# Kernel tuning notes

Measured on AMD Instinct MI355X. Metric: run time of the kernel, lower is better.

The kernel has to match this reference:

```python
import jax, jax.numpy as jnp
import numpy as np

N_NODES = 100_000
N_EDGES = 1_600_000
HIDDEN = 64
EPS = 1e-5  # eqx.nn.RMSNorm default eps


def setup_inputs() -> dict:
    key = jax.random.key(0)
    k1, k2, k3 = jax.random.split(key, 3)
    x = jax.random.normal(k1, (N_NODES, HIDDEN), dtype=jnp.float32)
    # edges[0] = target node i, edges[1] = source node j  (a[i, j] = 1 => edge j -> i)
    edges = jax.random.randint(k2, (2, N_EDGES), 0, N_NODES, dtype=jnp.int32)
    W = jax.random.normal(k3, (HIDDEN, HIDDEN), dtype=jnp.float32) * (1.0 / np.sqrt(HIDDEN))
    b = jnp.zeros((HIDDEN,), dtype=jnp.float32)
    norm_weight = jnp.ones((HIDDEN,), dtype=jnp.float32)
    norm_bias = jnp.zeros((HIDDEN,), dtype=jnp.float32)
    return {"x": x, "edges": edges, "W": W, "b": b,
            "norm_weight": norm_weight, "norm_bias": norm_bias}


def reference(x, edges, W, b, norm_weight, norm_bias):
    n_nodes = x.shape[0]
    # vmap(Linear) + relu:  m = relu(x @ W.T + b)
    m = jax.nn.relu(jnp.einsum('nd,kd->nk', x, W) + b)
    # a @ m : sum-aggregate messages from source j into target i
    dst, src = edges[0], edges[1]
    agg = jax.ops.segment_sum(m[src], dst, num_segments=n_nodes)
    # residual + RMSNorm (per-node)
    h = x + agg
    inv_rms = jax.lax.rsqrt(jnp.mean(h * h, axis=-1, keepdims=True) + EPS)
    return norm_weight * (h * inv_rms) + norm_bias
```

## Files before the change

### kernel.cpp

```cpp
#include <hip/hip_runtime.h>
#include <hip/hip_bf16.h>

#define N_NODES 100000
#define N_EDGES 1600000
#define HID 64

#define NG 196
#define GROUPS 511
#define GSTRIDE 512
#define NREP 2
#define RCAP 2048
#define EPT 16
#define BIN_BLOCKS 391
#define LIN_BLOCKS 1563
#define LCAP 48

using bf16 = __hip_bfloat16;
typedef __attribute__((ext_vector_type(8))) short short8;
typedef __attribute__((ext_vector_type(4))) float float4v;

__device__ __forceinline__ float bfbits2f(unsigned short u) {
    union { unsigned int i; float f; } v;
    v.i = ((unsigned int)u) << 16;
    return v.f;
}
__device__ __forceinline__ unsigned short f2bfbits(float f) {
    union { float f; unsigned int i; } v;
    v.f = f;
    unsigned int r = v.i + 0x7fffu + ((v.i >> 16) & 1u);
    return (unsigned short)(r >> 16);
}

__global__ __launch_bounds__(256) void k_init(
    const float* __restrict__ W, int* __restrict__ gcur,
    unsigned short* __restrict__ Wfhi, unsigned short* __restrict__ Wflo)
{
    const int t = blockIdx.x * 256 + threadIdx.x;
    for (int i = t; i < NREP * GSTRIDE; i += 512) gcur[i] = 0;
    for (int o = t; o < HID * HID; o += 512) {
        const int j = o & 7, l = (o >> 3) & 63, ksnt = o >> 9;
        const int ks = ksnt & 1, nt = ksnt >> 1;
        const int c = l & 15, q = l >> 4;
        const float f = W[(size_t)(nt * 16 + c) * HID + ks * 32 + q * 8 + j];
        const unsigned short h = f2bfbits(f);
        Wfhi[o] = h;
        Wflo[o] = f2bfbits(f - bfbits2f(h));
    }
}

__global__ __launch_bounds__(256, 4) void k_prep2(
    const float* __restrict__ x, const unsigned short* __restrict__ Wfhi,
    const unsigned short* __restrict__ Wflo, const float* __restrict__ b,
    bf16* __restrict__ m,
    const int* __restrict__ edges, int* __restrict__ gcur,
    int* __restrict__ binned)
{
    __shared__ union SM {
        struct { float xs[64 * 65]; } lin;
        struct { int cnt[GSTRIDE]; int base[GSTRIDE]; } bin;
    } sm;
    const int t = threadIdx.x;

    if (blockIdx.x < LIN_BLOCKS) {
        const int nb0 = blockIdx.x * 64;
        const float4* xg = reinterpret_cast<const float4*>(x) + (size_t)nb0 * 16;
        #pragma unroll
        for (int k = 0; k < 4; ++k) {
            const int f4 = t + k * 256;
            float4 v = make_float4(0.f, 0.f, 0.f, 0.f);
            if (nb0 * 16 + f4 < N_NODES * 16) v = xg[f4];
            const int r = f4 >> 4, fc = (f4 & 15) * 4;
            float* dst = &sm.lin.xs[r * 65 + fc];
            dst[0] = v.x; dst[1] = v.y; dst[2] = v.z; dst[3] = v.w;
        }
        __syncthreads();

        const int wv = t >> 6, l = t & 63;
        const int c = l & 15, q = l >> 4;
        const int tile = blockIdx.x * 4 + wv;
        if (tile >= N_NODES / 16) return;
        const int nb = tile * 16;

        const short8* wfh = reinterpret_cast<const short8*>(Wfhi);
        const short8* wfl = reinterpret_cast<const short8*>(Wflo);
        short8 Bhi[4][2], Blo[4][2];
        #pragma unroll
        for (int nt = 0; nt < 4; ++nt)
            #pragma unroll
            for (int ks = 0; ks < 2; ++ks) {
                const int fi = (nt * 2 + ks) * 64 + l;
                Bhi[nt][ks] = wfh[fi];
                Blo[nt][ks] = wfl[fi];
            }

        short8 Ahi[2];
        #pragma unroll
        for (int ks = 0; ks < 2; ++ks) {
            const float* xsrc = &sm.lin.xs[(wv * 16 + c) * 65 + ks * 32 + q * 8];
            #pragma unroll
            for (int j = 0; j < 8; ++j)
                Ahi[ks][j] = (short)f2bfbits(xsrc[j]);
        }

        float4v acc[4];
        #pragma unroll
        for (int nt = 0; nt < 4; ++nt) {
            const float bias = b[nt * 16 + c];
            acc[nt] = (float4v){bias, bias, bias, bias};
            #pragma unroll
            for (int ks = 0; ks < 2; ++ks) {
                acc[nt] = __builtin_amdgcn_mfma_f32_16x16x32_bf16(Ahi[ks], Bhi[nt][ks], acc[nt], 0, 0, 0);
                acc[nt] = __builtin_amdgcn_mfma_f32_16x16x32_bf16(Ahi[ks], Blo[nt][ks], acc[nt], 0, 0, 0);
            }
        }

        unsigned short* mp = reinterpret_cast<unsigned short*>(m);
        #pragma unroll
        for (int nt = 0; nt < 4; ++nt)
            #pragma unroll
            for (int rg = 0; rg < 4; ++rg) {
                const float v = fmaxf(acc[nt][rg], 0.0f);
                mp[(size_t)(nb + q * 4 + rg) * HID + nt * 16 + c] = f2bfbits(v);
            }
    } else {
        int* cnt  = sm.bin.cnt;
        int* base = sm.bin.base;
        const int bb = blockIdx.x - LIN_BLOCKS;
        for (int i = t; i < GSTRIDE; i += 256) cnt[i] = 0;
        __syncthreads();

        const int e0 = bb * (256 * EPT);
        int gk[EPT], pk[EPT], sl[EPT];
        #pragma unroll
        for (int k = 0; k < EPT; ++k) {
            const int e = e0 + k * 256 + t;
            if (e < N_EDGES) {
                const int dst = edges[e];
                const int src = edges[N_EDGES + e];
                const int g = (int)((unsigned)dst / NG);
                gk[k] = g;
                pk[k] = ((dst - g * NG) << 17) | src;
                sl[k] = atomicAdd(&cnt[g], 1);
            } else gk[k] = -1;
        }
        __syncthreads();
        const int r = bb & (NREP - 1);
        for (int i = t; i < GROUPS; i += 256) {
            const int cc = cnt[i];
            base[i] = cc ? atomicAdd(&gcur[r * GSTRIDE + i], cc) : 0;
        }
        __syncthreads();
        #pragma unroll
        for (int k = 0; k < EPT; ++k) {
            if (gk[k] >= 0) {
                const int pos = base[gk[k]] + sl[k];
                if ((unsigned)pos < RCAP)
                    binned[(size_t)(r * GSTRIDE + gk[k]) * RCAP + pos] = pk[k];
            }
        }
    }
}

__global__ __launch_bounds__(1024, 8) void k_gather_norm6(
    const float* __restrict__ x, const bf16* __restrict__ m,
    const int* __restrict__ gcur, const int* __restrict__ binned,
    const float* __restrict__ nw, const float* __restrict__ nb,
    float* __restrict__ out)
{
    __shared__ int lcount[NG];
    __shared__ int lsrc[NG * LCAP];
    const int t = threadIdx.x;
    const int g = blockIdx.x;
    for (int i = t; i < NG; i += 1024) lcount[i] = 0;
    __syncthreads();

    #pragma unroll
    for (int rr = 0; rr < NREP; ++rr) {
        int c = gcur[rr * GSTRIDE + g];
        if (c > RCAP) c = RCAP;
        const int* reg = binned + (size_t)(rr * GSTRIDE + g) * RCAP;
        for (int i = t; i < c; i += 1024) {
            const int pr = reg[i];
            const int dl = pr >> 17;
            const int slot = atomicAdd(&lcount[dl], 1);
            if (slot < LCAP) lsrc[dl * LCAP + slot] = pr & 0x1FFFF;
        }
    }
    __syncthreads();

    const int wv = t >> 6, l = t & 63;
    const int c = l & 15;
    const int r = l >> 4;
    const ushort4* mu4 = reinterpret_cast<const ushort4*>(m);
    const float4 nw4 = reinterpret_cast<const float4*>(nw)[c];
    const float4 nb4 = reinterpret_cast<const float4*>(nb)[c];

    for (int dl = wv; dl < NG; dl += 16) {
        const int n = g * NG + dl;
        if (n >= N_NODES) break;
        int deg = lcount[dl]; if (deg > LCAP) deg = LCAP;
        const int* row = &lsrc[dl * LCAP];

        float4 a = make_float4(0.f, 0.f, 0.f, 0.f);
        for (int i0 = 0; i0 < deg; i0 += 32) {
            ushort4 vb[8];
            #pragma unroll
            for (int j = 0; j < 8; ++j) {
                const int e = i0 + j * 4 + r;
                const int ec = (e < deg) ? e : (deg - 1);
                vb[j] = mu4[(size_t)row[ec] * 16 + c];
            }
            #pragma unroll
            for (int j = 0; j < 8; ++j) {
                const int e = i0 + j * 4 + r;
                if (e < deg) {
                    a.x += bfbits2f(vb[j].x);
                    a.y += bfbits2f(vb[j].y);
                    a.z += bfbits2f(vb[j].z);
                    a.w += bfbits2f(vb[j].w);
                }
            }
        }
        a.x += __shfl_xor(a.x, 16, 64); a.x += __shfl_xor(a.x, 32, 64);
        a.y += __shfl_xor(a.y, 16, 64); a.y += __shfl_xor(a.y, 32, 64);
        a.z += __shfl_xor(a.z, 16, 64); a.z += __shfl_xor(a.z, 32, 64);
        a.w += __shfl_xor(a.w, 16, 64); a.w += __shfl_xor(a.w, 32, 64);

        const float4 x4 = reinterpret_cast<const float4*>(x)[(size_t)n * 16 + c];
        float4 h;
        h.x = x4.x + a.x; h.y = x4.y + a.y; h.z = x4.z + a.z; h.w = x4.w + a.w;
        float ss = h.x * h.x + h.y * h.y + h.z * h.z + h.w * h.w;
        ss += __shfl_xor(ss, 1, 64);
        ss += __shfl_xor(ss, 2, 64);
        ss += __shfl_xor(ss, 4, 64);
        ss += __shfl_xor(ss, 8, 64);
        const float inv = rsqrtf(ss * (1.0f / HID) + 1e-5f);
        if (r == 0) {
            float4 o;
            o.x = nw4.x * h.x * inv + nb4.x;
            o.y = nw4.y * h.y * inv + nb4.y;
            o.z = nw4.z * h.z * inv + nb4.z;
            o.w = nw4.w * h.w * inv + nb4.w;
            reinterpret_cast<float4*>(out)[(size_t)n * 16 + c] = o;
        }
    }
}

extern "C" void kernel_launch(void* const* d_in, const int* in_sizes, int n_in,
                              void* d_out, int out_size, void* d_ws, size_t ws_size,
                              hipStream_t stream) {
    const float* x     = (const float*)d_in[0];
    const int*   edges = (const int*)d_in[1];
    const float* W     = (const float*)d_in[2];
    const float* b     = (const float*)d_in[3];
    const float* nw    = (const float*)d_in[4];
    const float* nb    = (const float*)d_in[5];
    float* out = (float*)d_out;

    int* gcur = (int*)d_ws;
    unsigned short* Wfhi = (unsigned short*)((char*)d_ws + (1 << 14));
    unsigned short* Wflo = Wfhi + HID * HID;
    int*  binned = (int*)((char*)d_ws + (1 << 16));
    bf16* m      = (bf16*)((char*)d_ws + (1 << 16) +
                           (size_t)NREP * GSTRIDE * RCAP * sizeof(int));

    k_init<<<2, 256, 0, stream>>>(W, gcur, Wfhi, Wflo);
    k_prep2<<<LIN_BLOCKS + BIN_BLOCKS, 256, 0, stream>>>(x, Wfhi, Wflo, b, m, edges, gcur, binned);
    k_gather_norm6<<<GROUPS, 1024, 0, stream>>>(x, m, gcur, binned, nw, nb, out);
}
```

Measured before the change: 149.6 us.

## Aggregate neighbor messages with one-hot bf16 MFMA over 16-node tiles

The gather kernel now buckets edges into tiles of 16 destination nodes instead of per-node lists. Each wave loads source message rows as 16-byte vectors, transposes them through LDS with ds_read_b64_tr_b16, and sums them into the destination nodes with a one-hot bf16 MFMA. The goal is to replace per-lane scalar bf16-to-float adds and shuffle reductions with matrix-core accumulation, and to use wider loads. In exchange there is extra LDS staging, padding waste per 32-edge chunk, and a smaller block (768 threads) whose per-tile capacity limit could drop edges.

```diff
diff --git a/kernel.cpp b/kernel.cpp
--- a/kernel.cpp
+++ b/kernel.cpp
@@ -13,10 +13,15 @@
 #define EPT 16
 #define BIN_BLOCKS 391
 #define LIN_BLOCKS 1563
-#define LCAP 48
+
+#define TILES 13
+#define TCAP 384
+#define GTHREADS 768
+#define GWAVES 12
 
 using bf16 = __hip_bfloat16;
 typedef __attribute__((ext_vector_type(8))) short short8;
+typedef __attribute__((ext_vector_type(4))) short short4v;
 typedef __attribute__((ext_vector_type(4))) float float4v;
 
 __device__ __forceinline__ float bfbits2f(unsigned short u) {
@@ -161,17 +166,23 @@
     }
 }
 
-__global__ __launch_bounds__(1024, 8) void k_gather_norm6(
+#define TRREAD(dst, OFF) \
+    asm volatile("ds_read_b64_tr_b16 %0, %1 offset:" #OFF \
+                 : "=v"(dst) : "v"(traddr) : "memory")
+
+__global__ __launch_bounds__(GTHREADS, 6) void k_gather_mfma(
     const float* __restrict__ x, const bf16* __restrict__ m,
     const int* __restrict__ gcur, const int* __restrict__ binned,
-    const float* __restrict__ nw, const float* __restrict__ nb,
+    const float* __restrict__ nw, const float* __restrict__ nbias,
     float* __restrict__ out)
 {
-    __shared__ int lcount[NG];
-    __shared__ int lsrc[NG * LCAP];
+    __shared__ int tcnt[TILES];
+    __shared__ int tlist[TILES * TCAP];
+    __shared__ uint4 stg4[GWAVES * 128];
+
     const int t = threadIdx.x;
     const int g = blockIdx.x;
-    for (int i = t; i < NG; i += 1024) lcount[i] = 0;
+    if (t < TILES) tcnt[t] = 0;
     __syncthreads();
 
     #pragma unroll
@@ -179,69 +190,125 @@
         int c = gcur[rr * GSTRIDE + g];
         if (c > RCAP) c = RCAP;
         const int* reg = binned + (size_t)(rr * GSTRIDE + g) * RCAP;
-        for (int i = t; i < c; i += 1024) {
+        for (int i = t; i < c; i += GTHREADS) {
             const int pr = reg[i];
-            const int dl = pr >> 17;
-            const int slot = atomicAdd(&lcount[dl], 1);
-            if (slot < LCAP) lsrc[dl * LCAP + slot] = pr & 0x1FFFF;
+            const int tile = pr >> 21;
+            const int slot = atomicAdd(&tcnt[tile], 1);
+            if (slot < TCAP) tlist[tile * TCAP + slot] = pr & 0x1FFFFF;
         }
     }
     __syncthreads();
 
     const int wv = t >> 6, l = t & 63;
-    const int c = l & 15;
-    const int r = l >> 4;
-    const ushort4* mu4 = reinterpret_cast<const ushort4*>(m);
-    const float4 nw4 = reinterpret_cast<const float4*>(nw)[c];
-    const float4 nb4 = reinterpret_cast<const float4*>(nb)[c];
-
-    for (int dl = wv; dl < NG; dl += 16) {
+    const int q = l >> 4;
+    const int node16 = l & 15;
+    const int fq = l & 7;
+    const int sr = l >> 3;
+    const int stg_c = ((fq >> 1) << 9) | ((l >> 5) << 7) | ((sr & 3) << 5) | ((l & 1) << 4);
+    const int kq0 = ((sr >> 2) << 3) + (sr & 3);
+    const int kq1 = (((sr + 8) >> 2) << 3) + (sr & 3);
+    char* stg_wave = (char*)(&stg4[0]) + (wv << 11);
+    const unsigned traddr = (unsigned)(size_t)stg_wave + (unsigned)(l << 3);
+    const uint4* mv = reinterpret_cast<const uint4*>(m);
+
+    for (int tile = wv; tile < TILES; tile += GWAVES) {
+        int K = tcnt[tile];
+        if (K > TCAP) K = TCAP;
+        const int lbase = tile * TCAP;
+        float4v acc0 = {0.f, 0.f, 0.f, 0.f};
+        float4v acc1 = acc0, acc2 = acc0, acc3 = acc0;
+        const int nch = (K + 31) >> 5;
+
+        for (int ch = 0; ch < nch; ++ch) {
+            const int k0 = ch << 5;
+            const int kA0 = k0 + kq0, kA1 = k0 + kq1;
+            const int tA0i = (kA0 < K) ? tlist[lbase + kA0] : 0;
+            const int tA1i = (kA1 < K) ? tlist[lbase + kA1] : 0;
+            const int tB0i = (kA0 + 4 < K) ? tlist[lbase + kA0 + 4] : 0;
+            const int tB1i = (kA1 + 4 < K) ? tlist[lbase + kA1 + 4] : 0;
+            const uint4 vA0 = mv[(size_t)(tA0i & 0x1FFFF) * 8 + fq];
+            const uint4 vA1 = mv[(size_t)(tA1i & 0x1FFFF) * 8 + fq];
+            const uint4 vB0 = mv[(size_t)(tB0i & 0x1FFFF) * 8 + fq];
+            const uint4 vB1 = mv[(size_t)(tB1i & 0x1FFFF) * 8 + fq];
+
+            *reinterpret_cast<uint4*>(stg_wave + stg_c) = vA0;
+            *reinterpret_cast<uint4*>(stg_wave + stg_c + 256) = vA1;
+            short4v tA0, tA1, tA2, tA3;
+            TRREAD(tA0, 0); TRREAD(tA1, 512); TRREAD(tA2, 1024); TRREAD(tA3, 1536);
+
+            *reinterpret_cast<uint4*>(stg_wave + stg_c) = vB0;
+            *reinterpret_cast<uint4*>(stg_wave + stg_c + 256) = vB1;
+            short4v tB0, tB1, tB2, tB3;
+            TRREAD(tB0, 0); TRREAD(tB1, 512); TRREAD(tB2, 1024); TRREAD(tB3, 1536);
+
+            const int kb = k0 + (q << 3);
+            short8 bh;
+            #pragma unroll
+            for (int jj = 0; jj < 8; ++jj) {
+                const int kk = kb + jj;
+                const int tb = (kk < K) ? tlist[lbase + kk] : -1;
+                bh[jj] = (short)(((tb >> 17) == node16) ? 0x3F80 : 0);
+            }
+
+            asm volatile("s_waitcnt lgkmcnt(0)" ::: "memory");
+            __builtin_amdgcn_sched_barrier(0);
+            const short8 a0 = __builtin_shufflevector(tA0, tB0, 0, 1, 2, 3, 4, 5, 6, 7);
+            const short8 a1 = __builtin_shufflevector(tA1, tB1, 0, 1, 2, 3, 4, 5, 6, 7);
+            const short8 a2 = __builtin_shufflevector(tA2, tB2, 0, 1, 2, 3, 4, 5, 6, 7);
+            const short8 a3 = __builtin_shufflevector(tA3, tB3, 0, 1, 2, 3, 4, 5, 6, 7);
+            acc0 = __builtin_amdgcn_mfma_f32_16x16x32_bf16(a0, bh, acc0, 0, 0, 0);
+            acc1 = __builtin_amdgcn_mfma_f32_16x16x32_bf16(a1, bh, acc1, 0, 0, 0);
+            acc2 = __builtin_amdgcn_mfma_f32_16x16x32_bf16(a2, bh, acc2, 0, 0, 0);
+            acc3 = __builtin_amdgcn_mfma_f32_16x16x32_bf16(a3, bh, acc3, 0, 0, 0);
+        }
+
+        const int dl = (tile << 4) + node16;
         const int n = g * NG + dl;
-        if (n >= N_NODES) break;
-        int deg = lcount[dl]; if (deg > LCAP) deg = LCAP;
-        const int* row = &lsrc[dl * LCAP];
-
-        float4 a = make_float4(0.f, 0.f, 0.f, 0.f);
-        for (int i0 = 0; i0 < deg; i0 += 32) {
-            ushort4 vb[8];
-            #pragma unroll
-            for (int j = 0; j < 8; ++j) {
-                const int e = i0 + j * 4 + r;
-                const int ec = (e < deg) ? e : (deg - 1);
-                vb[j] = mu4[(size_t)row[ec] * 16 + c];
-            }
-            #pragma unroll
-            for (int j = 0; j < 8; ++j) {
-                const int e = i0 + j * 4 + r;
-                if (e < deg) {
-                    a.x += bfbits2f(vb[j].x);
-                    a.y += bfbits2f(vb[j].y);
-                    a.z += bfbits2f(vb[j].z);
-                    a.w += bfbits2f(vb[j].w);
-                }
-            }
-        }
-        a.x += __shfl_xor(a.x, 16, 64); a.x += __shfl_xor(a.x, 32, 64);
-        a.y += __shfl_xor(a.y, 16, 64); a.y += __shfl_xor(a.y, 32, 64);
-        a.z += __shfl_xor(a.z, 16, 64); a.z += __shfl_xor(a.z, 32, 64);
-        a.w += __shfl_xor(a.w, 16, 64); a.w += __shfl_xor(a.w, 32, 64);
-
-        const float4 x4 = reinterpret_cast<const float4*>(x)[(size_t)n * 16 + c];
-        float4 h;
-        h.x = x4.x + a.x; h.y = x4.y + a.y; h.z = x4.z + a.z; h.w = x4.w + a.w;
-        float ss = h.x * h.x + h.y * h.y + h.z * h.z + h.w * h.w;
-        ss += __shfl_xor(ss, 1, 64);
-        ss += __shfl_xor(ss, 2, 64);
-        ss += __shfl_xor(ss, 4, 64);
-        ss += __shfl_xor(ss, 8, 64);
-        const float inv = rsqrtf(ss * (1.0f / HID) + 1e-5f);
-        if (r == 0) {
-            float4 o;
-            o.x = nw4.x * h.x * inv + nb4.x;
-            o.y = nw4.y * h.y * inv + nb4.y;
-            o.z = nw4.z * h.z * inv + nb4.z;
-            o.w = nw4.w * h.w * inv + nb4.w;
-            reinterpret_cast<float4*>(out)[(size_t)n * 16 + c] = o;
+        if (dl < NG && n < N_NODES) {
+            const float4* xr = reinterpret_cast<const float4*>(x) + (size_t)n * 16 + q;
+            const float4 x0 = xr[0], x1 = xr[4], x2 = xr[8], x3 = xr[12];
+            const float h00 = x0.x + acc0[0], h01 = x0.y + acc0[1], h02 = x0.z + acc0[2], h03 = x0.w + acc0[3];
+            const float h10 = x1.x + acc1[0], h11 = x1.y + acc1[1], h12 = x1.z + acc1[2], h13 = x1.w + acc1[3];
+            const float h20 = x2.x + acc2[0], h21 = x2.y + acc2[1], h22 = x2.z + acc2[2], h23 = x2.w + acc2[3];
+            const float h30 = x3.x + acc3[0], h31 = x3.y + acc3[1], h32 = x3.z + acc3[2], h33 = x3.w + acc3[3];
+            float ss = h00 * h00 + h01 * h01 + h02 * h02 + h03 * h03
+                     + h10 * h10 + h11 * h11 + h12 * h12 + h13 * h13
+                     + h20 * h20 + h21 * h21 + h22 * h22 + h23 * h23
+                     + h30 * h30 + h31 * h31 + h32 * h32 + h33 * h33;
+            ss += __shfl_xor(ss, 16, 64);
+            ss += __shfl_xor(ss, 32, 64);
+            const float inv = rsqrtf(ss * (1.0f / HID) + 1e-5f);
+            const float4* nwp = reinterpret_cast<const float4*>(nw);
+            const float4* nbp = reinterpret_cast<const float4*>(nbias);
+            float4* op = reinterpret_cast<float4*>(out) + (size_t)n * 16 + q;
+            {
+                const float4 w = nwp[q], bb = nbp[q];
+                float4 o;
+                o.x = w.x * h00 * inv + bb.x; o.y = w.y * h01 * inv + bb.y;
+                o.z = w.z * h02 * inv + bb.z; o.w = w.w * h03 * inv + bb.w;
+                op[0] = o;
+            }
+            {
+                const float4 w = nwp[4 + q], bb = nbp[4 + q];
+                float4 o;
+                o.x = w.x * h10 * inv + bb.x; o.y = w.y * h11 * inv + bb.y;
+                o.z = w.z * h12 * inv + bb.z; o.w = w.w * h13 * inv + bb.w;
+                op[4] = o;
+            }
+            {
+                const float4 w = nwp[8 + q], bb = nbp[8 + q];
+                float4 o;
+                o.x = w.x * h20 * inv + bb.x; o.y = w.y * h21 * inv + bb.y;
+                o.z = w.z * h22 * inv + bb.z; o.w = w.w * h23 * inv + bb.w;
+                op[8] = o;
+            }
+            {
+                const float4 w = nwp[12 + q], bb = nbp[12 + q];
+                float4 o;
+                o.x = w.x * h30 * inv + bb.x; o.y = w.y * h31 * inv + bb.y;
+                o.z = w.z * h32 * inv + bb.z; o.w = w.w * h33 * inv + bb.w;
+                op[12] = o;
+            }
         }
     }
 }
@@ -266,5 +333,5 @@
 
     k_init<<<2, 256, 0, stream>>>(W, gcur, Wfhi, Wflo);
     k_prep2<<<LIN_BLOCKS + BIN_BLOCKS, 256, 0, stream>>>(x, Wfhi, Wflo, b, m, edges, gcur, binned);
-    k_gather_norm6<<<GROUPS, 1024, 0, stream>>>(x, m, gcur, binned, nw, nb, out);
-}
+    k_gather_mfma<<<GROUPS, GTHREADS, 0, stream>>>(x, m, gcur, binned, nw, nb, out);
+}
```

Result: faster. 143.2 us (-4.3%).
